# Optimization experiments

Measured on AMD Instinct MI355X. Metric: run time of the kernel, lower is better.

Reference implementation:

```python
import jax, jax.numpy as jnp
import numpy as np

DT = 0.001  # forward's default dt
EPS = 1e-10


def setup_inputs() -> dict:
    key = jax.random.key(0)
    k1, k2 = jax.random.split(key)
    nt, ntr, nc = 4096, 1024, 3
    x = jax.random.normal(k1, (nt, ntr, nc), dtype=jnp.float32)
    y = jax.random.normal(k2, (nt, ntr, nc), dtype=jnp.float32)
    return {"x": x, "y": y}


def reference(x, y):
    # x, y: [nt, ntraces, nchannels]
    nt = x.shape[0]
    # autocorrelation energy per (trace, channel) column via Parseval-style FFT sum
    X = jnp.fft.fft(x, axis=0)
    Y = jnp.fft.fft(y, axis=0)
    Ex = DT * jnp.sum(jnp.abs(X) ** 2, axis=0) / nt + EPS  # [ntr, nc]
    Ey = DT * jnp.sum(jnp.abs(Y) ** 2, axis=0) / nt + EPS  # [ntr, nc]
    dots = jnp.sum(x * y, axis=0)                          # [ntr, nc]
    cc = dots / jnp.sqrt(Ex * Ey)                          # [ntr, nc]
    # original skips columns whose max |x| is exactly 0
    mask = jnp.max(jnp.abs(x), axis=0) > 0
    loss = jnp.sum(jnp.where(mask, cc, 0.0))
    return loss
```

## Files before the change

### kernel.cpp

```cpp
#include <hip/hip_runtime.h>


#define NT 4096
#define NCOL 3072
#define NCOL4 768
#define CHUNKS 256
#define TSTEPS (NT / CHUNKS)
#define BATCH 8

typedef float vfloat4 __attribute__((ext_vector_type(4)));

#define PS_F4_PER_STAT (CHUNKS * NCOL4)

__global__ __launch_bounds__(256, 3) void ncc_stage1(const float* __restrict__ x,
                                                     const float* __restrict__ y,
                                                     float* __restrict__ ws) {
    const int bx   = blockIdx.x;
    const int g    = bx % 3;
    const int ch   = bx / 3;
    const int tid  = threadIdx.x;
    const int col4 = g * 256 + tid;

    const vfloat4* __restrict__ x4 =
        reinterpret_cast<const vfloat4*>(x) + (size_t)ch * TSTEPS * NCOL4 + col4;
    const vfloat4* __restrict__ y4 =
        reinterpret_cast<const vfloat4*>(y) + (size_t)ch * TSTEPS * NCOL4 + col4;
    vfloat4* __restrict__ ps = reinterpret_cast<vfloat4*>(ws);

    vfloat4 sx2 = {0.f, 0.f, 0.f, 0.f};
    vfloat4 sy2 = {0.f, 0.f, 0.f, 0.f};
    vfloat4 sxy = {0.f, 0.f, 0.f, 0.f};

#pragma unroll
    for (int b = 0; b < TSTEPS / BATCH; ++b) {
        vfloat4 xv[BATCH], yv[BATCH];
#pragma unroll
        for (int i = 0; i < BATCH; ++i) {
            const int t = b * BATCH + i;
            xv[i] = __builtin_nontemporal_load(x4 + t * NCOL4);
            yv[i] = __builtin_nontemporal_load(y4 + t * NCOL4);
        }
#pragma unroll
        for (int i = 0; i < BATCH; ++i) {
            sx2 = xv[i] * xv[i] + sx2;
            sy2 = yv[i] * yv[i] + sy2;
            sxy = xv[i] * yv[i] + sxy;
        }
    }

    const int slot = ch * NCOL4 + col4;
    ps[0 * PS_F4_PER_STAT + slot] = sx2;
    ps[1 * PS_F4_PER_STAT + slot] = sy2;
    ps[2 * PS_F4_PER_STAT + slot] = sxy;
}

__global__ __launch_bounds__(256) void ncc_stage2(const float* __restrict__ ws,
                                                  float* __restrict__ out) {
    const int b    = blockIdx.x;
    const int tid  = threadIdx.x;
    const int lane = tid & 63;
    const int q    = tid >> 6;
    const int j    = b * 64 + lane;

    float sx2 = 0.f, sy2 = 0.f, sxy = 0.f;
    const int c0 = q * (CHUNKS / 4);
#pragma unroll 8
    for (int c = c0; c < c0 + CHUNKS / 4; ++c) {
        sx2 += ws[0 * CHUNKS * NCOL + c * NCOL + j];
        sy2 += ws[1 * CHUNKS * NCOL + c * NCOL + j];
        sxy += ws[2 * CHUNKS * NCOL + c * NCOL + j];
    }

    __shared__ float red[3][4][64];
    red[0][q][lane] = sx2;
    red[1][q][lane] = sy2;
    red[2][q][lane] = sxy;
    __syncthreads();

    if (q == 0) {
        sx2 = red[0][0][lane] + red[0][1][lane] + red[0][2][lane] + red[0][3][lane];
        sy2 = red[1][0][lane] + red[1][1][lane] + red[1][2][lane] + red[1][3][lane];
        sxy = red[2][0][lane] + red[2][1][lane] + red[2][2][lane] + red[2][3][lane];
        float ex = fmaf(0.001f, sx2, 1e-10f);
        float ey = fmaf(0.001f, sy2, 1e-10f);
        float cc = (sx2 > 0.f) ? sxy * rsqrtf(ex * ey) : 0.f;
#pragma unroll
        for (int off = 32; off > 0; off >>= 1)
            cc += __shfl_down(cc, off, 64);
        if (lane == 0)
            atomicAdd(out, cc);
    }
}

extern "C" void kernel_launch(void* const* d_in, const int* in_sizes, int n_in,
                              void* d_out, int out_size, void* d_ws, size_t ws_size,
                              hipStream_t stream) {
    const float* x = reinterpret_cast<const float*>(d_in[0]);
    const float* y = reinterpret_cast<const float*>(d_in[1]);
    float* out = reinterpret_cast<float*>(d_out);
    float* ws = reinterpret_cast<float*>(d_ws);

    ncc_stage1<<<dim3(3 * CHUNKS), dim3(256), 0, stream>>>(x, y, ws);
    ncc_stage2<<<dim3(48), dim3(256), 0, stream>>>(ws, out);
}
```

Baseline: 124.3 us.

## Reduce time chunks in-block via LDS and shrink partial-sum workspace

Stage 1 blocks now cover 64 columns (float4) across 64 time steps. Each wave takes 16 time steps, and the block combines the waves' partials through shared memory before writing. This cuts the workspace from 256 to 64 partial chunks, so stage 2 reads less and the workspace write traffic drops. Nontemporal loads are replaced with ordinary loads, which may change cache behaviour. Each wave now reads a 1 KB contiguous segment per row instead of 4 KB per block row, so access locality changes.

```diff
diff --git a/kernel.cpp b/kernel.cpp
--- a/kernel.cpp
+++ b/kernel.cpp
@@ -4,41 +4,44 @@
 #define NT 4096
 #define NCOL 3072
 #define NCOL4 768
-#define CHUNKS 256
-#define TSTEPS (NT / CHUNKS)
+#define CGROUPS 12
+#define TCHUNKS 64
+#define WTS 16
 #define BATCH 8
 
 typedef float vfloat4 __attribute__((ext_vector_type(4)));
 
-#define PS_F4_PER_STAT (CHUNKS * NCOL4)
+#define PS_STRIDE_STAT (TCHUNKS * NCOL)
 
 __global__ __launch_bounds__(256, 3) void ncc_stage1(const float* __restrict__ x,
                                                      const float* __restrict__ y,
                                                      float* __restrict__ ws) {
     const int bx   = blockIdx.x;
-    const int g    = bx % 3;
-    const int ch   = bx / 3;
+    const int cg   = bx % CGROUPS;
+    const int tc   = bx / CGROUPS;
     const int tid  = threadIdx.x;
-    const int col4 = g * 256 + tid;
+    const int w    = tid >> 6;
+    const int lane = tid & 63;
+    const int col4 = cg * 64 + lane;
 
+    const int tbase = tc * 64 + w * WTS;
     const vfloat4* __restrict__ x4 =
-        reinterpret_cast<const vfloat4*>(x) + (size_t)ch * TSTEPS * NCOL4 + col4;
+        reinterpret_cast<const vfloat4*>(x) + (size_t)tbase * NCOL4 + col4;
     const vfloat4* __restrict__ y4 =
-        reinterpret_cast<const vfloat4*>(y) + (size_t)ch * TSTEPS * NCOL4 + col4;
-    vfloat4* __restrict__ ps = reinterpret_cast<vfloat4*>(ws);
+        reinterpret_cast<const vfloat4*>(y) + (size_t)tbase * NCOL4 + col4;
 
     vfloat4 sx2 = {0.f, 0.f, 0.f, 0.f};
     vfloat4 sy2 = {0.f, 0.f, 0.f, 0.f};
     vfloat4 sxy = {0.f, 0.f, 0.f, 0.f};
 
 #pragma unroll
-    for (int b = 0; b < TSTEPS / BATCH; ++b) {
+    for (int b = 0; b < WTS / BATCH; ++b) {
         vfloat4 xv[BATCH], yv[BATCH];
 #pragma unroll
         for (int i = 0; i < BATCH; ++i) {
             const int t = b * BATCH + i;
-            xv[i] = __builtin_nontemporal_load(x4 + t * NCOL4);
-            yv[i] = __builtin_nontemporal_load(y4 + t * NCOL4);
+            xv[i] = x4[t * NCOL4];
+            yv[i] = y4[t * NCOL4];
         }
 #pragma unroll
         for (int i = 0; i < BATCH; ++i) {
@@ -48,10 +51,17 @@
         }
     }
 
-    const int slot = ch * NCOL4 + col4;
-    ps[0 * PS_F4_PER_STAT + slot] = sx2;
-    ps[1 * PS_F4_PER_STAT + slot] = sy2;
-    ps[2 * PS_F4_PER_STAT + slot] = sxy;
+    __shared__ vfloat4 red[3][4][64];
+    red[0][w][lane] = sx2;
+    red[1][w][lane] = sy2;
+    red[2][w][lane] = sxy;
+    __syncthreads();
+
+    if (w < 3) {
+        vfloat4 s = red[w][0][lane] + red[w][1][lane] + red[w][2][lane] + red[w][3][lane];
+        vfloat4* __restrict__ ps = reinterpret_cast<vfloat4*>(ws);
+        ps[(w * TCHUNKS + tc) * NCOL4 + col4] = s;
+    }
 }
 
 __global__ __launch_bounds__(256) void ncc_stage2(const float* __restrict__ ws,
@@ -63,12 +73,12 @@
     const int j    = b * 64 + lane;
 
     float sx2 = 0.f, sy2 = 0.f, sxy = 0.f;
-    const int c0 = q * (CHUNKS / 4);
-#pragma unroll 8
-    for (int c = c0; c < c0 + CHUNKS / 4; ++c) {
-        sx2 += ws[0 * CHUNKS * NCOL + c * NCOL + j];
-        sy2 += ws[1 * CHUNKS * NCOL + c * NCOL + j];
-        sxy += ws[2 * CHUNKS * NCOL + c * NCOL + j];
+    const int c0 = q * (TCHUNKS / 4);
+#pragma unroll
+    for (int c = c0; c < c0 + TCHUNKS / 4; ++c) {
+        sx2 += ws[0 * PS_STRIDE_STAT + c * NCOL + j];
+        sy2 += ws[1 * PS_STRIDE_STAT + c * NCOL + j];
+        sxy += ws[2 * PS_STRIDE_STAT + c * NCOL + j];
     }
 
     __shared__ float red[3][4][64];
@@ -100,6 +110,6 @@
     float* out = reinterpret_cast<float*>(d_out);
     float* ws = reinterpret_cast<float*>(d_ws);
 
-    ncc_stage1<<<dim3(3 * CHUNKS), dim3(256), 0, stream>>>(x, y, ws);
+    ncc_stage1<<<dim3(CGROUPS * TCHUNKS), dim3(256), 0, stream>>>(x, y, ws);
     ncc_stage2<<<dim3(48), dim3(256), 0, stream>>>(ws, out);
 }
```

New measurement: 114.3 us. 8.0% less time.
